# Performance work log

Measured on AMD Instinct MI355X. Metric: run time of the kernel, lower is better.

The kernel has to match this reference:

```python
import jax, jax.numpy as jnp
import numpy as np

QMIN, QMAX = -128.0, 127.0  # int8 range

def setup_inputs() -> dict:
    key = jax.random.key(0)
    k1, k2 = jax.random.split(key)
    B, S, D_IN, D_OUT = 4, 2048, 4096, 4096
    x = jax.random.normal(k1, (B, S, D_IN), dtype=jnp.float32)
    # int8 weight stored as int32 (values in int8 range)
    weight = jax.random.randint(k2, (D_OUT, D_IN), -128, 128, dtype=jnp.int32)
    scale = jnp.array([0.02], dtype=jnp.float32)        # per-tensor weight scale
    input_scale = jnp.array([0.05], dtype=jnp.float32)  # static activation scale
    return {"x": x, "weight": weight, "scale": scale, "input_scale": input_scale}

def reference(x, weight, scale, input_scale):
    # quantize_static_quant_activations: round(x/input_scale) clamped to int8 range,
    # then direct_cast_dequantize back to fp32 (kept as fp32 here; values are integral).
    x_q = jnp.clip(jnp.round(x / input_scale), QMIN, QMAX)
    # direct_cast_dequantize(weight) -> fp32
    w = weight.astype(jnp.float32)
    # F.linear: x_q @ w.T  -> [B, S, D_OUT]
    out = jnp.einsum('bsi,oi->bso', x_q, w)
    # scale_dequantize with combined scale = input_scale * weight_scale
    return out * (input_scale * scale)
```

## Files before the change

kernel.cpp:

```cpp
#include <hip/hip_runtime.h>
#include <stdint.h>

typedef int v4i __attribute__((ext_vector_type(4)));

static constexpr int MDIM = 8192;
static constexpr int NDIM = 4096;
static constexpr int KDIM = 4096;

static constexpr int QBLOCKS = (MDIM * KDIM / 16) / 256;
static constexpr int WBLOCKS = (NDIM * KDIM / 16) / 256;

__device__ __forceinline__ void lds_load16(const void* gptr, void* lptr) {
    __builtin_amdgcn_global_load_lds(
        (const __attribute__((address_space(1))) void*)(uintptr_t)gptr,
        (__attribute__((address_space(3))) void*)(uint32_t)(uintptr_t)lptr,
        16, 0, 0);
}

__device__ __forceinline__ int q1(float f, float s) {
    return (int)fminf(fmaxf(__builtin_rintf(f / s), -128.0f), 127.0f);
}
__device__ __forceinline__ int pack4(int a, int b, int c, int d) {
    return (a & 0xff) | ((b & 0xff) << 8) | ((c & 0xff) << 16) | ((d & 0xff) << 24);
}

__global__ __launch_bounds__(256) void prep_k(const float4* __restrict__ x,
                                              int4* __restrict__ xq,
                                              const int4* __restrict__ w,
                                              int4* __restrict__ wq,
                                              const float* __restrict__ s_in) {
    const int b = blockIdx.x;
    if (b < QBLOCKS) {
        const int i = b * 256 + threadIdx.x;
        const float s = s_in[0];
        const float4 v0 = x[4 * i + 0];
        const float4 v1 = x[4 * i + 1];
        const float4 v2 = x[4 * i + 2];
        const float4 v3 = x[4 * i + 3];
        int4 o;
        o.x = pack4(q1(v0.x, s), q1(v0.y, s), q1(v0.z, s), q1(v0.w, s));
        o.y = pack4(q1(v1.x, s), q1(v1.y, s), q1(v1.z, s), q1(v1.w, s));
        o.z = pack4(q1(v2.x, s), q1(v2.y, s), q1(v2.z, s), q1(v2.w, s));
        o.w = pack4(q1(v3.x, s), q1(v3.y, s), q1(v3.z, s), q1(v3.w, s));
        xq[i] = o;
    } else {
        const int i = (b - QBLOCKS) * 256 + threadIdx.x;
        const int4 a = w[4 * i + 0];
        const int4 c = w[4 * i + 1];
        const int4 d = w[4 * i + 2];
        const int4 e = w[4 * i + 3];
        int4 o;
        o.x = pack4(a.x, a.y, a.z, a.w);
        o.y = pack4(c.x, c.y, c.z, c.w);
        o.z = pack4(d.x, d.y, d.z, d.w);
        o.w = pack4(e.x, e.y, e.z, e.w);
        wq[i] = o;
    }
}

__global__ __launch_bounds__(512, 2) void gemm_i8_k(const int8_t* __restrict__ A,
                                                    const int8_t* __restrict__ Bt,
                                                    float* __restrict__ C,
                                                    const float* __restrict__ w_scale,
                                                    const float* __restrict__ in_scale) {
    __shared__ int8_t lds[131072];

    const int tid  = threadIdx.x;
    const int lane = tid & 63;
    const int wave = tid >> 6;
    const int wr = wave >> 2;
    const int wc = wave & 3;
    const int lm = lane & 15;
    const int q  = lane >> 4;

    const int bid = blockIdx.x;
    const int xcd = bid & 7;
    const int j   = bid >> 3;
    const int bm  = (xcd >> 1) * 8 + (j >> 3);
    const int bn  = (xcd & 1) * 8 + (j & 7);

    const int srow  = tid >> 2;
    const int sperm = ((tid & 3) ^ ((tid >> 3) & 3)) << 4;
    const int8_t* gA = A  + (size_t)(bm * 256 + srow) * KDIM + sperm;
    const int8_t* gB = Bt + (size_t)(bn * 256 + srow) * KDIM + sperm;
    const int ldsT = tid * 16;

#define STAGE(MATBASE, GSRC, slot, ks, kbyte)                                              \
    lds_load16(GSRC + (kbyte) + (ks) * 64,                                                 \
               lds + (MATBASE) + (slot) * 32768 + (ks) * 16384 + ldsT);                    \
    lds_load16(GSRC + (kbyte) + (ks) * 64 + 524288,                                        \
               lds + (MATBASE) + (slot) * 32768 + (ks) * 16384 + 8192 + ldsT);

    const int fsw = ((q ^ ((lm >> 1) & 3)) << 4);
    const int aB = (wr * 128 + lm) * 64 + fsw;
    const int bB = 65536 + (wc * 64 + lm) * 64 + fsw;

    v4i acc[8][4] = {{}};
    v4i av[4], bv[4];

#define RD(off) (*(const v4i*)(lds + (off)))

#define PHASE(slot, ks, mh, STAGES, VMW)                                                   \
    {                                                                                      \
        if ((mh) == 0) {                                                                   \
            bv[0] = RD(bB + (slot) * 32768 + (ks) * 16384 + 0 * 1024);                     \
            bv[1] = RD(bB + (slot) * 32768 + (ks) * 16384 + 1 * 1024);                     \
            bv[2] = RD(bB + (slot) * 32768 + (ks) * 16384 + 2 * 1024);                     \
            bv[3] = RD(bB + (slot) * 32768 + (ks) * 16384 + 3 * 1024);                     \
        }                                                                                  \
        av[0] = RD(aB + (slot) * 32768 + (ks) * 16384 + (mh) * 4096 + 0 * 1024);           \
        av[1] = RD(aB + (slot) * 32768 + (ks) * 16384 + (mh) * 4096 + 1 * 1024);           \
        av[2] = RD(aB + (slot) * 32768 + (ks) * 16384 + (mh) * 4096 + 2 * 1024);           \
        av[3] = RD(aB + (slot) * 32768 + (ks) * 16384 + (mh) * 4096 + 3 * 1024);           \
        STAGES                                                                             \
        __builtin_amdgcn_s_barrier();                                                      \
        asm volatile("s_waitcnt lgkmcnt(0)" ::: "memory");                                 \
        __builtin_amdgcn_s_setprio(1);                                                     \
        _Pragma("unroll")                                                                  \
        for (int mt = 0; mt < 4; ++mt)                                                     \
            _Pragma("unroll")                                                              \
            for (int nt = 0; nt < 4; ++nt)                                                 \
                acc[(mh) * 4 + mt][nt] = __builtin_amdgcn_mfma_i32_16x16x64_i8(            \
                    av[mt], bv[nt], acc[(mh) * 4 + mt][nt], 0, 0, 0);                      \
        __builtin_amdgcn_s_setprio(0);                                                     \
        VMW                                                                                \
        __builtin_amdgcn_s_barrier();                                                      \
    }

#define VM4 asm volatile("s_waitcnt vmcnt(4)" ::: "memory");
#define VM0 asm volatile("s_waitcnt vmcnt(0)" ::: "memory");

    STAGE(0, gA, 0, 0, 0) STAGE(65536, gB, 0, 0, 0)
    STAGE(0, gA, 0, 1, 0) STAGE(65536, gB, 0, 1, 0)
    STAGE(0, gA, 1, 0, 128) STAGE(65536, gB, 1, 0, 128)
    VM4
    __builtin_amdgcn_s_barrier();

#pragma unroll 1
    for (int i = 0; i < 15; ++i) {
        const int kb = i * 256;
        PHASE(0, 0, 0, STAGE(0, gA, 1, 1, kb + 128), )
        PHASE(0, 0, 1, STAGE(65536, gB, 1, 1, kb + 128), )
        PHASE(0, 1, 0, STAGE(0, gA, 0, 0, kb + 256), )
        PHASE(0, 1, 1, STAGE(65536, gB, 0, 0, kb + 256), VM4)
        PHASE(1, 0, 0, STAGE(0, gA, 0, 1, kb + 256), )
        PHASE(1, 0, 1, STAGE(65536, gB, 0, 1, kb + 256), )
        PHASE(1, 1, 0, STAGE(0, gA, 1, 0, kb + 384), )
        PHASE(1, 1, 1, STAGE(65536, gB, 1, 0, kb + 384), VM4)
    }
    PHASE(0, 0, 0, STAGE(0, gA, 1, 1, 3968), )
    PHASE(0, 0, 1, STAGE(65536, gB, 1, 1, 3968), )
    PHASE(0, 1, 0, , )
    PHASE(0, 1, 1, , VM0)
    PHASE(1, 0, 0, , )
    PHASE(1, 0, 1, , )
    PHASE(1, 1, 0, , )
    PHASE(1, 1, 1, , )

    const float fs = w_scale[0] * in_scale[0];
    float* Cb = C + (size_t)(bm * 256 + wr * 128 + q * 4) * NDIM + bn * 256 + wc * 64 + lm;
#pragma unroll
    for (int m = 0; m < 8; ++m)
#pragma unroll
        for (int n = 0; n < 4; ++n)
#pragma unroll
            for (int r = 0; r < 4; ++r)
                Cb[(size_t)(m * 16 + r) * NDIM + n * 16] = (float)acc[m][n][r] * fs;

#undef STAGE
#undef RD
#undef PHASE
#undef VM4
#undef VM0
}

extern "C" void kernel_launch(void* const* d_in, const int* in_sizes, int n_in,
                              void* d_out, int out_size, void* d_ws, size_t ws_size,
                              hipStream_t stream) {
    const float* x        = (const float*)d_in[0];
    const int*   w        = (const int*)d_in[1];
    const float* w_scale  = (const float*)d_in[2];
    const float* in_scale = (const float*)d_in[3];
    float* out = (float*)d_out;

    int8_t* xq = (int8_t*)d_ws;
    int8_t* wq = xq + (size_t)MDIM * KDIM;

    prep_k<<<QBLOCKS + WBLOCKS, 256, 0, stream>>>(
        (const float4*)x, (int4*)xq, (const int4*)w, (int4*)wq, in_scale);

    gemm_i8_k<<<512, 512, 0, stream>>>(xq, wq, out, w_scale, in_scale);
}
```

Baseline: 389.7 us.

## Switch int8 GEMM to 32x32x32 MFMA with split-K LDS reads per span

Replaces the 16x16x64 int8 MFMA tiling with 32x32x32 MFMA tiles, so each wave holds 4x2 v16i accumulators instead of 8x4 v4i. The main loop is restructured from four half-M phases per k-step pair into one span per 64-byte k-slice. Each span issues both A and B global-to-LDS stages and splits its LDS fragment reads into two halves, so the second half's reads overlap the first half's MFMAs, with adjusted vmcnt waits. The aim is fewer LDS reads per MFMA and fewer barriers. The risk is in the new swizzle and XOR offsets and the output row mapping for the 32x32 layout.

Result: slower. 406.8 us (+4.4%).

```diff
diff --git a/kernel.cpp b/kernel.cpp
--- a/kernel.cpp
+++ b/kernel.cpp
@@ -1,7 +1,8 @@
 #include <hip/hip_runtime.h>
 #include <stdint.h>
 
-typedef int v4i __attribute__((ext_vector_type(4)));
+typedef int v4i  __attribute__((ext_vector_type(4)));
+typedef int v16i __attribute__((ext_vector_type(16)));
 
 static constexpr int MDIM = 8192;
 static constexpr int NDIM = 4096;
@@ -70,8 +71,8 @@
     const int wave = tid >> 6;
     const int wr = wave >> 2;
     const int wc = wave & 3;
-    const int lm = lane & 15;
-    const int q  = lane >> 4;
+    const int lr = lane & 31;
+    const int h  = lane >> 5;
 
     const int bid = blockIdx.x;
     const int xcd = bid & 7;
@@ -91,85 +92,94 @@
     lds_load16(GSRC + (kbyte) + (ks) * 64 + 524288,                                        \
                lds + (MATBASE) + (slot) * 32768 + (ks) * 16384 + 8192 + ldsT);
 
-    const int fsw = ((q ^ ((lm >> 1) & 3)) << 4);
-    const int aB = (wr * 128 + lm) * 64 + fsw;
-    const int bB = 65536 + (wc * 64 + lm) * 64 + fsw;
-
-    v4i acc[8][4] = {{}};
-    v4i av[4], bv[4];
+    const int sw0 = ((h ^ ((lr >> 1) & 3)) << 4);
+    const int aO0 = (wr * 128 + lr) * 64 + sw0;
+    const int aO1 = aO0 ^ 32;
+    const int bO0 = 65536 + (wc * 64 + lr) * 64 + sw0;
+    const int bO1 = bO0 ^ 32;
+
+    v16i acc[4][2] = {{}};
+    v4i a0[4], a1[4], b0[2], b1[2];
 
 #define RD(off) (*(const v4i*)(lds + (off)))
-
-#define PHASE(slot, ks, mh, STAGES, VMW)                                                   \
+#define VM8 asm volatile("s_waitcnt vmcnt(8)" ::: "memory");
+#define VM4 asm volatile("s_waitcnt vmcnt(4)" ::: "memory");
+#define VM0 asm volatile("s_waitcnt vmcnt(0)" ::: "memory");
+
+#define SPAN(slot, ks, STA, STB, VMW)                                                      \
     {                                                                                      \
-        if ((mh) == 0) {                                                                   \
-            bv[0] = RD(bB + (slot) * 32768 + (ks) * 16384 + 0 * 1024);                     \
-            bv[1] = RD(bB + (slot) * 32768 + (ks) * 16384 + 1 * 1024);                     \
-            bv[2] = RD(bB + (slot) * 32768 + (ks) * 16384 + 2 * 1024);                     \
-            bv[3] = RD(bB + (slot) * 32768 + (ks) * 16384 + 3 * 1024);                     \
-        }                                                                                  \
-        av[0] = RD(aB + (slot) * 32768 + (ks) * 16384 + (mh) * 4096 + 0 * 1024);           \
-        av[1] = RD(aB + (slot) * 32768 + (ks) * 16384 + (mh) * 4096 + 1 * 1024);           \
-        av[2] = RD(aB + (slot) * 32768 + (ks) * 16384 + (mh) * 4096 + 2 * 1024);           \
-        av[3] = RD(aB + (slot) * 32768 + (ks) * 16384 + (mh) * 4096 + 3 * 1024);           \
-        STAGES                                                                             \
-        __builtin_amdgcn_s_barrier();                                                      \
-        asm volatile("s_waitcnt lgkmcnt(0)" ::: "memory");                                 \
+        constexpr int RG = (slot) * 32768 + (ks) * 16384;                                  \
+        a0[0] = RD(aO0 + RG + 0 * 2048);                                                   \
+        a0[1] = RD(aO0 + RG + 1 * 2048);                                                   \
+        a0[2] = RD(aO0 + RG + 2 * 2048);                                                   \
+        a0[3] = RD(aO0 + RG + 3 * 2048);                                                   \
+        b0[0] = RD(bO0 + RG + 0 * 2048);                                                   \
+        b0[1] = RD(bO0 + RG + 1 * 2048);                                                   \
+        __builtin_amdgcn_sched_barrier(0);          \
+        STA                                                                                \
+        a1[0] = RD(aO1 + RG + 0 * 2048);                                                   \
+        a1[1] = RD(aO1 + RG + 1 * 2048);                                                   \
+        a1[2] = RD(aO1 + RG + 2 * 2048);                                                   \
+        a1[3] = RD(aO1 + RG + 3 * 2048);                                                   \
+        b1[0] = RD(bO1 + RG + 0 * 2048);                                                   \
+        b1[1] = RD(bO1 + RG + 1 * 2048);                                                   \
+        STB                                                                                \
+        asm volatile("s_waitcnt lgkmcnt(6)" ::: "memory");     \
+        __builtin_amdgcn_sched_barrier(0);                                                 \
         __builtin_amdgcn_s_setprio(1);                                                     \
         _Pragma("unroll")                                                                  \
         for (int mt = 0; mt < 4; ++mt)                                                     \
             _Pragma("unroll")                                                              \
-            for (int nt = 0; nt < 4; ++nt)                                                 \
-                acc[(mh) * 4 + mt][nt] = __builtin_amdgcn_mfma_i32_16x16x64_i8(            \
-                    av[mt], bv[nt], acc[(mh) * 4 + mt][nt], 0, 0, 0);                      \
+            for (int nt = 0; nt < 2; ++nt)                                                 \
+                acc[mt][nt] = __builtin_amdgcn_mfma_i32_32x32x32_i8(                       \
+                    a0[mt], b0[nt], acc[mt][nt], 0, 0, 0);                                 \
+        asm volatile("s_waitcnt lgkmcnt(0)" ::: "memory");   \
+        __builtin_amdgcn_sched_barrier(0);                                                 \
+        _Pragma("unroll")                                                                  \
+        for (int mt = 0; mt < 4; ++mt)                                                     \
+            _Pragma("unroll")                                                              \
+            for (int nt = 0; nt < 2; ++nt)                                                 \
+                acc[mt][nt] = __builtin_amdgcn_mfma_i32_32x32x32_i8(                       \
+                    a1[mt], b1[nt], acc[mt][nt], 0, 0, 0);                                 \
         __builtin_amdgcn_s_setprio(0);                                                     \
         VMW                                                                                \
         __builtin_amdgcn_s_barrier();                                                      \
     }
 
-#define VM4 asm volatile("s_waitcnt vmcnt(4)" ::: "memory");
-#define VM0 asm volatile("s_waitcnt vmcnt(0)" ::: "memory");
-
     STAGE(0, gA, 0, 0, 0) STAGE(65536, gB, 0, 0, 0)
     STAGE(0, gA, 0, 1, 0) STAGE(65536, gB, 0, 1, 0)
     STAGE(0, gA, 1, 0, 128) STAGE(65536, gB, 1, 0, 128)
-    VM4
+    VM8
     __builtin_amdgcn_s_barrier();
 
 #pragma unroll 1
-    for (int i = 0; i < 15; ++i) {
-        const int kb = i * 256;
-        PHASE(0, 0, 0, STAGE(0, gA, 1, 1, kb + 128), )
-        PHASE(0, 0, 1, STAGE(65536, gB, 1, 1, kb + 128), )
-        PHASE(0, 1, 0, STAGE(0, gA, 0, 0, kb + 256), )
-        PHASE(0, 1, 1, STAGE(65536, gB, 0, 0, kb + 256), VM4)
-        PHASE(1, 0, 0, STAGE(0, gA, 0, 1, kb + 256), )
-        PHASE(1, 0, 1, STAGE(65536, gB, 0, 1, kb + 256), )
-        PHASE(1, 1, 0, STAGE(0, gA, 1, 0, kb + 384), )
-        PHASE(1, 1, 1, STAGE(65536, gB, 1, 0, kb + 384), VM4)
+    for (int it = 0; it < 15; ++it) {
+        const int kb = it * 256;
+        SPAN(0, 0, STAGE(0, gA, 1, 1, kb + 128), STAGE(65536, gB, 1, 1, kb + 128), VM8)
+        SPAN(0, 1, STAGE(0, gA, 0, 0, kb + 256), STAGE(65536, gB, 0, 0, kb + 256), VM8)
+        SPAN(1, 0, STAGE(0, gA, 0, 1, kb + 256), STAGE(65536, gB, 0, 1, kb + 256), VM8)
+        SPAN(1, 1, STAGE(0, gA, 1, 0, kb + 384), STAGE(65536, gB, 1, 0, kb + 384), VM8)
     }
-    PHASE(0, 0, 0, STAGE(0, gA, 1, 1, 3968), )
-    PHASE(0, 0, 1, STAGE(65536, gB, 1, 1, 3968), )
-    PHASE(0, 1, 0, , )
-    PHASE(0, 1, 1, , VM0)
-    PHASE(1, 0, 0, , )
-    PHASE(1, 0, 1, , )
-    PHASE(1, 1, 0, , )
-    PHASE(1, 1, 1, , )
+    SPAN(0, 0, STAGE(0, gA, 1, 1, 3968), STAGE(65536, gB, 1, 1, 3968), VM8)
+    SPAN(0, 1, , , VM4)
+    SPAN(1, 0, , , VM0)
+    SPAN(1, 1, , , )
 
     const float fs = w_scale[0] * in_scale[0];
-    float* Cb = C + (size_t)(bm * 256 + wr * 128 + q * 4) * NDIM + bn * 256 + wc * 64 + lm;
+    float* Cb = C + (size_t)(bm * 256 + wr * 128 + h * 4) * NDIM + bn * 256 + wc * 64 + lr;
 #pragma unroll
-    for (int m = 0; m < 8; ++m)
+    for (int mt = 0; mt < 4; ++mt)
 #pragma unroll
-        for (int n = 0; n < 4; ++n)
+        for (int nt = 0; nt < 2; ++nt)
 #pragma unroll
-            for (int r = 0; r < 4; ++r)
-                Cb[(size_t)(m * 16 + r) * NDIM + n * 16] = (float)acc[m][n][r] * fs;
+            for (int r = 0; r < 16; ++r)
+                Cb[(size_t)(mt * 32 + (r & 3) + 8 * (r >> 2)) * NDIM + nt * 32] =
+                    (float)acc[mt][nt][r] * fs;
 
 #undef STAGE
 #undef RD
-#undef PHASE
+#undef SPAN
+#undef VM8
 #undef VM4
 #undef VM0
 }
```

## Double-buffer A-fragment LDS reads and drop pre-MFMA barrier in int8 GEMM

Applied to the files above, without the earlier changes.

Splits the A register fragments into two buffers so the next phase's LDS reads are issued before the current phase's MFMAs. This lets LDS latency overlap with matrix compute. The barrier before the MFMA block is removed and the wait becomes a partial lgkmcnt gate, with sched_barriers pinning the order. The global-load wait depth moves from vmcnt(4) to vmcnt(6), which keeps more prefetches in flight. The trade-offs are higher register pressure, and a risk of LDS races if the slot reuse timing across the single remaining barrier per phase is wrong.

Result: no change. 389.3 us (-0.1%).

```diff
diff --git a/kernel.cpp b/kernel.cpp
--- a/kernel.cpp
+++ b/kernel.cpp
@@ -96,81 +96,99 @@
     const int bB = 65536 + (wc * 64 + lm) * 64 + fsw;
 
     v4i acc[8][4] = {{}};
-    v4i av[4], bv[4];
+    v4i av[2][4], bv[4];
 
 #define RD(off) (*(const v4i*)(lds + (off)))
-
-#define PHASE(slot, ks, mh, STAGES, VMW)                                                   \
+#define RGN(slot, ks) ((slot) * 32768 + (ks) * 16384)
+
+#define PREF_AV(nb, slot, ks, mh)                                                          \
+    av[nb][0] = RD(aB + RGN(slot, ks) + (mh) * 4096 + 0);                                  \
+    av[nb][1] = RD(aB + RGN(slot, ks) + (mh) * 4096 + 1024);                               \
+    av[nb][2] = RD(aB + RGN(slot, ks) + (mh) * 4096 + 2048);                               \
+    av[nb][3] = RD(aB + RGN(slot, ks) + (mh) * 4096 + 3072);
+
+#define READ_BV(slot, ks)                                                                  \
+    bv[0] = RD(bB + RGN(slot, ks) + 0);                                                    \
+    bv[1] = RD(bB + RGN(slot, ks) + 1024);                                                 \
+    bv[2] = RD(bB + RGN(slot, ks) + 2048);                                                 \
+    bv[3] = RD(bB + RGN(slot, ks) + 3072);
+
+#define VM6 asm volatile("s_waitcnt vmcnt(6)" ::: "memory");
+#define VM4 asm volatile("s_waitcnt vmcnt(4)" ::: "memory");
+#define VM2 asm volatile("s_waitcnt vmcnt(2)" ::: "memory");
+#define VM0 asm volatile("s_waitcnt vmcnt(0)" ::: "memory");
+
+#define PHASE(mh, cb, BVR, PRF, STG, GATEN, VMW)                                           \
     {                                                                                      \
-        if ((mh) == 0) {                                                                   \
-            bv[0] = RD(bB + (slot) * 32768 + (ks) * 16384 + 0 * 1024);                     \
-            bv[1] = RD(bB + (slot) * 32768 + (ks) * 16384 + 1 * 1024);                     \
-            bv[2] = RD(bB + (slot) * 32768 + (ks) * 16384 + 2 * 1024);                     \
-            bv[3] = RD(bB + (slot) * 32768 + (ks) * 16384 + 3 * 1024);                     \
-        }                                                                                  \
-        av[0] = RD(aB + (slot) * 32768 + (ks) * 16384 + (mh) * 4096 + 0 * 1024);           \
-        av[1] = RD(aB + (slot) * 32768 + (ks) * 16384 + (mh) * 4096 + 1 * 1024);           \
-        av[2] = RD(aB + (slot) * 32768 + (ks) * 16384 + (mh) * 4096 + 2 * 1024);           \
-        av[3] = RD(aB + (slot) * 32768 + (ks) * 16384 + (mh) * 4096 + 3 * 1024);           \
-        STAGES                                                                             \
-        __builtin_amdgcn_s_barrier();                                                      \
-        asm volatile("s_waitcnt lgkmcnt(0)" ::: "memory");                                 \
+        BVR                                                                                \
+        PRF                                                                                \
+        STG                                                                                \
+        asm volatile("s_waitcnt lgkmcnt(" #GATEN ")" ::: "memory");                        \
+        __builtin_amdgcn_sched_barrier(0);                                                 \
         __builtin_amdgcn_s_setprio(1);                                                     \
         _Pragma("unroll")                                                                  \
         for (int mt = 0; mt < 4; ++mt)                                                     \
             _Pragma("unroll")                                                              \
             for (int nt = 0; nt < 4; ++nt)                                                 \
                 acc[(mh) * 4 + mt][nt] = __builtin_amdgcn_mfma_i32_16x16x64_i8(            \
-                    av[mt], bv[nt], acc[(mh) * 4 + mt][nt], 0, 0, 0);                      \
+                    av[cb][mt], bv[nt], acc[(mh) * 4 + mt][nt], 0, 0, 0);                  \
         __builtin_amdgcn_s_setprio(0);                                                     \
+        __builtin_amdgcn_sched_barrier(0);                                                 \
         VMW                                                                                \
         __builtin_amdgcn_s_barrier();                                                      \
     }
-
-#define VM4 asm volatile("s_waitcnt vmcnt(4)" ::: "memory");
-#define VM0 asm volatile("s_waitcnt vmcnt(0)" ::: "memory");
 
     STAGE(0, gA, 0, 0, 0) STAGE(65536, gB, 0, 0, 0)
     STAGE(0, gA, 0, 1, 0) STAGE(65536, gB, 0, 1, 0)
     STAGE(0, gA, 1, 0, 128) STAGE(65536, gB, 1, 0, 128)
-    VM4
+    asm volatile("s_waitcnt vmcnt(8)" ::: "memory");
     __builtin_amdgcn_s_barrier();
+    PREF_AV(0, 0, 0, 0)
 
 #pragma unroll 1
-    for (int i = 0; i < 15; ++i) {
-        const int kb = i * 256;
-        PHASE(0, 0, 0, STAGE(0, gA, 1, 1, kb + 128), )
-        PHASE(0, 0, 1, STAGE(65536, gB, 1, 1, kb + 128), )
-        PHASE(0, 1, 0, STAGE(0, gA, 0, 0, kb + 256), )
-        PHASE(0, 1, 1, STAGE(65536, gB, 0, 0, kb + 256), VM4)
-        PHASE(1, 0, 0, STAGE(0, gA, 0, 1, kb + 256), )
-        PHASE(1, 0, 1, STAGE(65536, gB, 0, 1, kb + 256), )
-        PHASE(1, 1, 0, STAGE(0, gA, 1, 0, kb + 384), )
-        PHASE(1, 1, 1, STAGE(65536, gB, 1, 0, kb + 384), VM4)
-    }
-    PHASE(0, 0, 0, STAGE(0, gA, 1, 1, 3968), )
-    PHASE(0, 0, 1, STAGE(65536, gB, 1, 1, 3968), )
-    PHASE(0, 1, 0, , )
-    PHASE(0, 1, 1, , VM0)
-    PHASE(1, 0, 0, , )
-    PHASE(1, 0, 1, , )
-    PHASE(1, 1, 0, , )
-    PHASE(1, 1, 1, , )
+    for (int it = 0; it < 15; ++it) {
+        const int kb = it * 256;
+        PHASE(0, 0, READ_BV(0, 0), PREF_AV(1, 0, 0, 1), STAGE(0, gA, 1, 1, kb + 128), 4, VM6)
+        PHASE(1, 1, ,               PREF_AV(0, 0, 1, 0), STAGE(65536, gB, 1, 1, kb + 128), 4, VM6)
+        PHASE(0, 0, READ_BV(0, 1), PREF_AV(1, 0, 1, 1), STAGE(0, gA, 0, 0, kb + 256), 4, VM6)
+        PHASE(1, 1, ,               PREF_AV(0, 1, 0, 0), STAGE(65536, gB, 0, 0, kb + 256), 4, VM6)
+        PHASE(0, 0, READ_BV(1, 0), PREF_AV(1, 1, 0, 1), STAGE(0, gA, 0, 1, kb + 256), 4, VM6)
+        PHASE(1, 1, ,               PREF_AV(0, 1, 1, 0), STAGE(65536, gB, 0, 1, kb + 256), 4, VM6)
+        PHASE(0, 0, READ_BV(1, 1), PREF_AV(1, 1, 1, 1), STAGE(0, gA, 1, 0, kb + 384), 4, VM6)
+        PHASE(1, 1, ,               PREF_AV(0, 0, 0, 0), STAGE(65536, gB, 1, 0, kb + 384), 4, VM6)
+    }
+    PHASE(0, 0, READ_BV(0, 0), PREF_AV(1, 0, 0, 1), STAGE(0, gA, 1, 1, 3968), 4, VM6)
+    PHASE(1, 1, ,               PREF_AV(0, 0, 1, 0), STAGE(65536, gB, 1, 1, 3968), 4, VM6)
+    PHASE(0, 0, READ_BV(0, 1), PREF_AV(1, 0, 1, 1), , 4, VM4)
+    PHASE(1, 1, ,               PREF_AV(0, 1, 0, 0), , 4, VM2)
+    PHASE(0, 0, READ_BV(1, 0), PREF_AV(1, 1, 0, 1), , 4, VM0)
+    PHASE(1, 1, ,               PREF_AV(0, 1, 1, 0), , 4, )
+    PHASE(0, 0, READ_BV(1, 1), PREF_AV(1, 1, 1, 1), , 4, )
+    PHASE(1, 1, ,               ,                    , 0, )
 
     const float fs = w_scale[0] * in_scale[0];
-    float* Cb = C + (size_t)(bm * 256 + wr * 128 + q * 4) * NDIM + bn * 256 + wc * 64 + lm;
+    const int crow = q * 4;
 #pragma unroll
-    for (int m = 0; m < 8; ++m)
+    for (int m = 0; m < 8; ++m) {
 #pragma unroll
-        for (int n = 0; n < 4; ++n)
+        for (int n = 0; n < 4; ++n) {
+            const size_t nn = (size_t)bn * 256 + wc * 64 + n * 16 + lm;
+            const size_t mb = (size_t)bm * 256 + wr * 128 + m * 16 + crow;
 #pragma unroll
             for (int r = 0; r < 4; ++r)
-                Cb[(size_t)(m * 16 + r) * NDIM + n * 16] = (float)acc[m][n][r] * fs;
+                C[(mb + r) * NDIM + nn] = (float)acc[m][n][r] * fs;
+        }
+    }
 
 #undef STAGE
 #undef RD
+#undef RGN
+#undef PREF_AV
+#undef READ_BV
 #undef PHASE
+#undef VM6
 #undef VM4
+#undef VM2
 #undef VM0
 }
 
@@ -189,5 +207,6 @@
     prep_k<<<QBLOCKS + WBLOCKS, 256, 0, stream>>>(
         (const float4*)x, (int4*)xq, (const int4*)w, (int4*)wq, in_scale);
 
-    gemm_i8_k<<<512, 512, 0, stream>>>(xq, wq, out, w_scale, in_scale);
-}
+    dim3 grid(512);
+    gemm_i8_k<<<grid, 512, 0, stream>>>(xq, wq, out, w_scale, in_scale);
+}
```
